# Performance work log

Hardware: AMD Instinct MI355X
Metric: run time of the kernel (lower is better)

## Reference

```python
import jax, jax.numpy as jnp
import numpy as np

T_STEPS = 1000
TEMP_SAMPLE = 0.1


def _cosine_schedule():
    # matches MBDDegradationImputation._cosine_beta_schedule (float64 then cast)
    s = 0.008
    x = np.linspace(0, T_STEPS, T_STEPS + 1, dtype=np.float64)
    ac = np.cos((x / T_STEPS + s) / (1 + s) * np.pi * 0.5) ** 2
    ac = ac / ac[0]
    betas = np.clip(1.0 - ac[1:] / ac[:-1], 0.0, 0.999)
    alphas = 1.0 - betas
    acp = np.cumprod(alphas)
    return (jnp.asarray(alphas, jnp.float32),
            jnp.asarray(acp, jnp.float32),
            jnp.asarray(np.sqrt(1.0 - acp), jnp.float32))


def setup_inputs() -> dict:
    key = jax.random.key(0)
    k = jax.random.split(key, 6)
    N, T, F = 2048, 512, 64
    Xbar_i = jax.random.normal(k[0], (T, F), jnp.float32)
    observed_data = jax.random.normal(k[1], (T, F), jnp.float32)
    time_points = jnp.linspace(0.0, 1.0, T, dtype=jnp.float32)
    mask = jax.random.uniform(k[2], (T, F)) > 0.3  # True = observed
    eps = jax.random.normal(k[3], (N, T, F), jnp.float32)
    deg_a = jax.random.normal(k[4], (F,), jnp.float32) * 0.1
    deg_b = jax.random.normal(k[5], (F,), jnp.float32) * 0.1
    return {"Xbar_i": Xbar_i, "observed_data": observed_data,
            "time_points": time_points, "mask": mask, "eps": eps,
            "deg_a": deg_a, "deg_b": deg_b, "i": 500}


def reference(Xbar_i, observed_data, time_points, mask, eps, deg_a, deg_b, i):
    alphas, acp, sigmas = _cosine_schedule()
    abar_i = acp[i]
    sigma_i = sigmas[i]
    alpha_i = alphas[i]
    abar_im1 = acp[i - 1]

    Yi = jnp.sqrt(abar_i) * Xbar_i  # (T, F)
    # candidate clean samples, clipped, observed positions restored
    X0s = jnp.clip(eps * sigma_i + Xbar_i, -1.0, 1.0)  # (N, T, F)
    cand = jnp.where(mask[None], observed_data[None], X0s)  # (N, T, F)

    # linear degradation model consistency: pred = a + b * t, score = -MSE
    pred = deg_a[None, :] + deg_b[None, :] * time_points[:, None]  # (T, F)
    scores = -jnp.mean((cand - pred[None]) ** 2, axis=(1, 2))  # (N,)

    std = jnp.maximum(jnp.std(scores, ddof=1), 1e-4)  # torch.std is unbiased
    logp0 = (scores - jnp.mean(scores)) / std / TEMP_SAMPLE
    weights = jax.nn.softmax(logp0)  # (N,)

    weighted = jnp.einsum('n,ntf->tf', weights, X0s)  # (T, F)
    # per-feature: missing positions get weighted combo; fully-observed
    # features are copied from observed_data; observed positions of
    # partially-missing features stay zero (faithful to the torch loop)
    feat_all = jnp.all(mask, axis=0)  # (F,)
    Xbar = jnp.where(~mask, weighted,
                     jnp.where(feat_all[None, :], observed_data, 0.0))

    score = (-Yi + jnp.sqrt(abar_i) * Xbar) / (1.0 - abar_i)
    Xim1 = (Yi + (1.0 - abar_i) * score) / jnp.sqrt(alpha_i)
    Xbar_im1 = Xim1 / jnp.sqrt(abar_im1)
    Xbar_im1 = jnp.where(mask, observed_data, Xbar_im1)
    return Xbar_im1
```

## Files before the change

### kernel.cpp

```cpp
#include <hip/hip_runtime.h>

typedef __attribute__((ext_vector_type(4))) int   i32x4;
typedef __attribute__((ext_vector_type(4))) float f32x4;

#define TF    32768
#define TF4   8192
#define NS    2048
#define WCUT  1e-9f

__device__ __forceinline__ i32x4 mload4(const void* mask, int isI32, int idx4) {
  if (isI32) return ((const i32x4*)mask)[idx4];
  unsigned int w = ((const unsigned int*)mask)[idx4];
  i32x4 r;
  r[0] = (int)(w & 0xFFu);
  r[1] = (int)((w >> 8) & 0xFFu);
  r[2] = (int)((w >> 16) & 0xFFu);
  r[3] = (int)((w >> 24) & 0xFFu);
  return r;
}

__device__ __forceinline__ double ac_fn(int t) {
  const double s = 0.008;
  double c = cos(((double)t / 1000.0 + s) / (1.0 + s) * 1.5707963267948966);
  return c * c;
}
__device__ __forceinline__ double alpha_fn(int t) {
  double beta = 1.0 - ac_fn(t + 1) / ac_fn(t);
  beta = beta < 0.0 ? 0.0 : (beta > 0.999 ? 0.999 : beta);
  return 1.0 - beta;
}

__launch_bounds__(256)
__global__ void k1a_sched(const int* __restrict__ ip,
                          const unsigned int* __restrict__ maskw,
                          float* __restrict__ wsc) {
  const int tid = threadIdx.x;
  __shared__ int badsh;
  if (tid == 0) badsh = 0;
  __syncthreads();
  int bad = 0;
  for (int k = tid; k < TF4; k += 256)
    if (maskw[k] > 1u) bad = 1;
  if (bad) atomicOr(&badsh, 1);

  const int i = ip[0];
  __shared__ double prod[256];
  double p = 1.0;
  for (int t = tid; t < i; t += 256) p *= alpha_fn(t);
  prod[tid] = p;
  __syncthreads();
  for (int s = 128; s > 0; s >>= 1) {
    if (tid < s) prod[tid] *= prod[tid + s];
    __syncthreads();
  }
  if (tid == 0) {
    double acp_im1 = prod[0];
    double ai = alpha_fn(i);
    double acp_i = acp_im1 * ai;
    wsc[0] = (float)sqrt(1.0 - acp_i);
    wsc[1] = (float)acp_i;
    wsc[2] = (float)ai;
    wsc[3] = (float)acp_im1;
    ((int*)wsc)[8] = badsh ? 0 : 1;
  }
}

__launch_bounds__(256)
__global__ void k1b_tables(const float* __restrict__ xbar,
                           const float* __restrict__ obs,
                           const void* __restrict__ mask,
                           const float* __restrict__ timep,
                           const float* __restrict__ dega,
                           const float* __restrict__ degb,
                           const float* __restrict__ wsc,
                           float* __restrict__ sc, float* __restrict__ xq,
                           float* __restrict__ pq, double* __restrict__ osum_part) {
  const int tid = threadIdx.x;
  const int pos4 = blockIdx.x * 256 + tid;
  const float sig = wsc[0];
  const int isI32 = ((const int*)wsc)[8];

  const int t  = pos4 >> 4;
  const int f0 = (pos4 << 2) & 63;
  const float tv = timep[t];
  f32x4 da = *(const f32x4*)(dega + f0);
  f32x4 db = *(const f32x4*)(degb + f0);
  f32x4 x  = ((const f32x4*)xbar)[pos4];
  f32x4 o  = ((const f32x4*)obs)[pos4];
  i32x4 m  = mload4(mask, isI32, pos4);

  f32x4 scv, xqv, pqv;
  float od2 = 0.f;
  #pragma unroll
  for (int c = 0; c < 4; ++c) {
    const float pr = fmaf(db[c], tv, da[c]);
    const bool mm = m[c] != 0;
    scv[c] = mm ? 0.f : sig;
    xqv[c] = mm ? 0.f : x[c];
    pqv[c] = mm ? 0.f : pr;
    float d = o[c] - pr;
    od2 += mm ? d * d : 0.f;
  }
  ((f32x4*)sc)[pos4] = scv;
  ((f32x4*)xq)[pos4] = xqv;
  ((f32x4*)pq)[pos4] = pqv;

  __shared__ double red[256];
  red[tid] = (double)od2;
  __syncthreads();
  for (int s = 128; s > 0; s >>= 1) {
    if (tid < s) red[tid] += red[tid + s];
    __syncthreads();
  }
  if (tid == 0) osum_part[blockIdx.x] = red[0];
}

__launch_bounds__(256)
__global__ void k2_scores(const float* __restrict__ eps,
                          const float* __restrict__ sc,
                          const float* __restrict__ xq,
                          const float* __restrict__ pq,
                          double* __restrict__ pscore) {
  const int tid = threadIdx.x;
  const int n0 = blockIdx.x * 4;
  const int kq = blockIdx.y;
  const int kbeg = kq * (TF4 / 4);
  const f32x4* e4 = (const f32x4*)eps;
  const f32x4* sc4 = (const f32x4*)sc;
  const f32x4* xq4 = (const f32x4*)xq;
  const f32x4* pq4 = (const f32x4*)pq;

  double acc[4] = {0.0, 0.0, 0.0, 0.0};
  #pragma unroll 2
  for (int k = kbeg + tid; k < kbeg + TF4 / 4; k += 512) {
    const int k1 = k + 256;
    f32x4 sv0 = sc4[k],  xv0 = xq4[k],  pv0 = pq4[k];
    f32x4 sv1 = sc4[k1], xv1 = xq4[k1], pv1 = pq4[k1];
    #pragma unroll
    for (int r = 0; r < 4; ++r) {
      const size_t row = (size_t)(n0 + r) * TF4;
      f32x4 e0 = e4[row + k];
      f32x4 e1 = e4[row + k1];
      float s = 0.f;
      #pragma unroll
      for (int c = 0; c < 4; ++c) {
        float v = fmaf(e0[c], sv0[c], xv0[c]);
        v = fminf(fmaxf(v, -1.f), 1.f);
        float d = v - pv0[c];
        s = fmaf(d, d, s);
      }
      #pragma unroll
      for (int c = 0; c < 4; ++c) {
        float v = fmaf(e1[c], sv1[c], xv1[c]);
        v = fminf(fmaxf(v, -1.f), 1.f);
        float d = v - pv1[c];
        s = fmaf(d, d, s);
      }
      acc[r] += (double)s;
    }
  }
  __shared__ double red[4 * 256];
  #pragma unroll
  for (int r = 0; r < 4; ++r) red[r * 256 + tid] = acc[r];
  __syncthreads();
  for (int s = 128; s > 0; s >>= 1) {
    if (tid < s) {
      #pragma unroll
      for (int r = 0; r < 4; ++r) red[r * 256 + tid] += red[r * 256 + tid + s];
    }
    __syncthreads();
  }
  if (tid < 4) pscore[kq * NS + n0 + tid] = red[tid * 256];
}

__launch_bounds__(256)
__global__ void k3_softmax(const double* __restrict__ pscore,
                           const double* __restrict__ osum_part,
                           float* __restrict__ wsc,
                           int* __restrict__ cidx, float* __restrict__ cw) {
  const int tid = threadIdx.x;
  __shared__ double red[256];

  double osum = 0.0;
  if (tid < 32) osum = osum_part[tid];
  red[tid] = osum; __syncthreads();
  for (int st = 128; st > 0; st >>= 1) { if (tid < st) red[tid] += red[tid + st]; __syncthreads(); }
  osum = red[0];
  __syncthreads();

  float s[8];
  #pragma unroll
  for (int j = 0; j < 8; ++j) {
    int n = tid + 256 * j;
    double t = pscore[n] + pscore[NS + n] + pscore[2 * NS + n] + pscore[3 * NS + n];
    s[j] = -(float)((t + osum) * (1.0 / 32768.0));
  }
  double t = 0.0;
  #pragma unroll
  for (int j = 0; j < 8; ++j) t += (double)s[j];
  red[tid] = t; __syncthreads();
  for (int st = 128; st > 0; st >>= 1) { if (tid < st) red[tid] += red[tid + st]; __syncthreads(); }
  const float mean = (float)(red[0] * (1.0 / 2048.0));
  __syncthreads();
  double v = 0.0;
  #pragma unroll
  for (int j = 0; j < 8; ++j) { float d = s[j] - mean; v += (double)d * (double)d; }
  red[tid] = v; __syncthreads();
  for (int st = 128; st > 0; st >>= 1) { if (tid < st) red[tid] += red[tid + st]; __syncthreads(); }
  float stdv = (float)sqrt(red[0] / 2047.0);
  stdv = fmaxf(stdv, 1e-4f);
  const float inv = 10.0f / stdv;
  float lp[8];
  double mx = -1e300;
  #pragma unroll
  for (int j = 0; j < 8; ++j) { lp[j] = (s[j] - mean) * inv; mx = fmax(mx, (double)lp[j]); }
  __syncthreads();
  red[tid] = mx; __syncthreads();
  for (int st = 128; st > 0; st >>= 1) { if (tid < st) red[tid] = fmax(red[tid], red[tid + st]); __syncthreads(); }
  const float M = (float)red[0];
  __syncthreads();
  float ev[8]; double es = 0.0;
  #pragma unroll
  for (int j = 0; j < 8; ++j) { ev[j] = expf(lp[j] - M); es += (double)ev[j]; }
  red[tid] = es; __syncthreads();
  for (int st = 128; st > 0; st >>= 1) { if (tid < st) red[tid] += red[tid + st]; __syncthreads(); }
  const float invS = (float)(1.0 / red[0]);

  float w[8]; int keep[8]; int c = 0;
  #pragma unroll
  for (int j = 0; j < 8; ++j) {
    w[j] = ev[j] * invS;
    keep[j] = w[j] > WCUT;
    c += keep[j];
  }
  __shared__ int cnt[256];
  cnt[tid] = c; __syncthreads();
  for (int off = 1; off < 256; off <<= 1) {
    int vv = (tid >= off) ? cnt[tid - off] : 0;
    __syncthreads();
    cnt[tid] += vv;
    __syncthreads();
  }
  int base = cnt[tid] - c;
  #pragma unroll
  for (int j = 0; j < 8; ++j) {
    if (keep[j]) {
      cidx[base] = tid + 256 * j;
      cw[base] = w[j];
      ++base;
    }
  }
  if (tid == 255) ((int*)wsc)[9] = cnt[255];
}

__launch_bounds__(256)
__global__ void k4_weighted(const float* __restrict__ eps,
                            const int* __restrict__ cidx,
                            const float* __restrict__ cw,
                            const float* __restrict__ wsc,
                            const float* __restrict__ xbar,
                            float* __restrict__ partial) {
  const int tid = threadIdx.x;
  const int pos4 = blockIdx.x * 256 + tid;
  const int g = blockIdx.y;
  const int Nk = ((const int*)wsc)[9];
  const float sig = wsc[0];
  const f32x4* e4 = (const f32x4*)eps;
  f32x4 xf = ((const f32x4*)xbar)[pos4];
  f32x4 acc = {0.f, 0.f, 0.f, 0.f};
  int j = g;
  for (; j + 16 < Nk; j += 32) {
    const float w0 = cw[j];
    const int   n0 = cidx[j];
    const float w1 = cw[j + 16];
    const int   n1 = cidx[j + 16];
    f32x4 e0 = e4[(size_t)n0 * TF4 + pos4];
    f32x4 e1 = e4[(size_t)n1 * TF4 + pos4];
    #pragma unroll
    for (int c = 0; c < 4; ++c) {
      float v = fmaf(e0[c], sig, xf[c]);
      v = fminf(fmaxf(v, -1.f), 1.f);
      acc[c] = fmaf(w0, v, acc[c]);
    }
    #pragma unroll
    for (int c = 0; c < 4; ++c) {
      float v = fmaf(e1[c], sig, xf[c]);
      v = fminf(fmaxf(v, -1.f), 1.f);
      acc[c] = fmaf(w1, v, acc[c]);
    }
  }
  for (; j < Nk; j += 16) {
    const float w = cw[j];
    const int n = cidx[j];
    f32x4 e = e4[(size_t)n * TF4 + pos4];
    #pragma unroll
    for (int c = 0; c < 4; ++c) {
      float v = fmaf(e[c], sig, xf[c]);
      v = fminf(fmaxf(v, -1.f), 1.f);
      acc[c] = fmaf(w, v, acc[c]);
    }
  }
  ((f32x4*)partial)[(size_t)g * TF4 + pos4] = acc;
}

__launch_bounds__(256)
__global__ void k5_final(const float* __restrict__ partial,
                         const float* __restrict__ xbar,
                         const float* __restrict__ obs,
                         const void* __restrict__ mask,
                         const float* __restrict__ wsc,
                         float* __restrict__ out) {
  const int pos4 = blockIdx.x * 256 + threadIdx.x;
  const f32x4* p4 = (const f32x4*)partial;
  f32x4 w = {0.f, 0.f, 0.f, 0.f};
  #pragma unroll
  for (int g = 0; g < 16; ++g) {
    f32x4 a = p4[(size_t)g * TF4 + pos4];
    #pragma unroll
    for (int c = 0; c < 4; ++c) w[c] += a[c];
  }
  const float abar = wsc[1];
  const float sa = sqrtf(abar);
  const float ra = 1.f / sqrtf(wsc[2]);
  const float rb = 1.f / sqrtf(wsc[3]);
  const int isI32 = ((const int*)wsc)[8];
  f32x4 xf = ((const f32x4*)xbar)[pos4];
  f32x4 ov = ((const f32x4*)obs)[pos4];
  i32x4 m = mload4(mask, isI32, pos4);
  f32x4 res;
  #pragma unroll
  for (int c = 0; c < 4; ++c) {
    const float Yi = sa * xf[c];
    const float scv = (-Yi + sa * w[c]) / (1.f - abar);
    const float xim1 = (Yi + (1.f - abar) * scv) * ra;
    res[c] = m[c] ? ov[c] : (xim1 * rb);
  }
  ((f32x4*)out)[pos4] = res;
}

extern "C" void kernel_launch(void* const* d_in, const int* in_sizes, int n_in,
                              void* d_out, int out_size, void* d_ws, size_t ws_size,
                              hipStream_t stream) {
  const float* Xbar  = (const float*)d_in[0];
  const float* obs   = (const float*)d_in[1];
  const float* timep = (const float*)d_in[2];
  const void*  mask  = d_in[3];
  const float* eps   = (const float*)d_in[4];
  const float* dega  = (const float*)d_in[5];
  const float* degb  = (const float*)d_in[6];
  const int*   ip    = (const int*)d_in[7];

  float* ws = (float*)d_ws;
  float*  wsc       = ws;
  float*  sc        = ws + 16;
  float*  xq        = sc + TF;
  float*  pq        = xq + TF;
  double* osum_part = (double*)(pq + TF);
  double* pscore    = osum_part + 32;
  int*    cidx      = (int*)(pscore + 4 * NS);
  float*  cw        = (float*)(cidx + NS);
  float*  partial   = cw + NS;

  hipLaunchKernelGGL(k1a_sched,  dim3(1),        dim3(256), 0, stream,
                     ip, (const unsigned int*)mask, wsc);
  hipLaunchKernelGGL(k1b_tables, dim3(32),       dim3(256), 0, stream,
                     Xbar, obs, mask, timep, dega, degb, wsc, sc, xq, pq, osum_part);
  hipLaunchKernelGGL(k2_scores,  dim3(NS/4, 4),  dim3(256), 0, stream,
                     eps, sc, xq, pq, pscore);
  hipLaunchKernelGGL(k3_softmax, dim3(1),        dim3(256), 0, stream,
                     pscore, osum_part, wsc, cidx, cw);
  hipLaunchKernelGGL(k4_weighted,dim3(32, 16),   dim3(256), 0, stream,
                     eps, cidx, cw, wsc, Xbar, partial);
  hipLaunchKernelGGL(k5_final,   dim3(32),       dim3(256), 0, stream,
                     partial, Xbar, obs, mask, wsc, (float*)d_out);
}
```

Before: 75.10 us.

## Fuse schedule and table kernels, fold observed residual into pq, widen weighted split

Merges the single-block schedule kernel into the table-building kernel. Each of the 32 blocks now recomputes the alpha cumulative product redundantly, which saves one launch and its dependency gap. The observed-position residual is folded into the pq table (obs - pred at masked positions), so k2 picks it up directly and the separate osum reduction and its k3 pre-pass go away. This relies on how k2, which is not shown, uses pq at masked entries. The weighted-sum kernel's grid is also doubled to 32 groups, adding parallelism at the cost of a larger partial buffer that k5 must read.

```diff
diff --git a/kernel.cpp b/kernel.cpp
--- a/kernel.cpp
+++ b/kernel.cpp
@@ -6,6 +6,7 @@
 #define TF    32768
 #define TF4   8192
 #define NS    2048
+#define NG    32
 #define WCUT  1e-9f
 
 __device__ __forceinline__ i32x4 mload4(const void* mask, int isI32, int idx4) {
@@ -31,11 +32,22 @@
 }
 
 __launch_bounds__(256)
-__global__ void k1a_sched(const int* __restrict__ ip,
-                          const unsigned int* __restrict__ maskw,
-                          float* __restrict__ wsc) {
+__global__ void k1_fused(const int* __restrict__ ip,
+                         const unsigned int* __restrict__ maskw,
+                         const float* __restrict__ timep,
+                         const float* __restrict__ dega,
+                         const float* __restrict__ degb,
+                         const float* __restrict__ xbar,
+                         const float* __restrict__ obs,
+                         const void* __restrict__ mask,
+                         float* __restrict__ wsc,
+                         float* __restrict__ sc, float* __restrict__ xq,
+                         float* __restrict__ pq) {
   const int tid = threadIdx.x;
   __shared__ int badsh;
+  __shared__ double prod[256];
+  __shared__ float ssig;
+  __shared__ int sIsI32;
   if (tid == 0) badsh = 0;
   __syncthreads();
   int bad = 0;
@@ -44,7 +56,6 @@
   if (bad) atomicOr(&badsh, 1);
 
   const int i = ip[0];
-  __shared__ double prod[256];
   double p = 1.0;
   for (int t = tid; t < i; t += 256) p *= alpha_fn(t);
   prod[tid] = p;
@@ -57,29 +68,22 @@
     double acp_im1 = prod[0];
     double ai = alpha_fn(i);
     double acp_i = acp_im1 * ai;
-    wsc[0] = (float)sqrt(1.0 - acp_i);
-    wsc[1] = (float)acp_i;
-    wsc[2] = (float)ai;
-    wsc[3] = (float)acp_im1;
-    ((int*)wsc)[8] = badsh ? 0 : 1;
-  }
-}
-
-__launch_bounds__(256)
-__global__ void k1b_tables(const float* __restrict__ xbar,
-                           const float* __restrict__ obs,
-                           const void* __restrict__ mask,
-                           const float* __restrict__ timep,
-                           const float* __restrict__ dega,
-                           const float* __restrict__ degb,
-                           const float* __restrict__ wsc,
-                           float* __restrict__ sc, float* __restrict__ xq,
-                           float* __restrict__ pq, double* __restrict__ osum_part) {
-  const int tid = threadIdx.x;
+    float sig = (float)sqrt(1.0 - acp_i);
+    ssig = sig;
+    sIsI32 = badsh ? 0 : 1;
+    if (blockIdx.x == 0) {
+      wsc[0] = sig;
+      wsc[1] = (float)acp_i;
+      wsc[2] = (float)ai;
+      wsc[3] = (float)acp_im1;
+      ((int*)wsc)[8] = badsh ? 0 : 1;
+    }
+  }
+  __syncthreads();
+  const float sig = ssig;
+  const int isI32 = sIsI32;
+
   const int pos4 = blockIdx.x * 256 + tid;
-  const float sig = wsc[0];
-  const int isI32 = ((const int*)wsc)[8];
-
   const int t  = pos4 >> 4;
   const int f0 = (pos4 << 2) & 63;
   const float tv = timep[t];
@@ -90,29 +94,17 @@
   i32x4 m  = mload4(mask, isI32, pos4);
 
   f32x4 scv, xqv, pqv;
-  float od2 = 0.f;
   #pragma unroll
   for (int c = 0; c < 4; ++c) {
     const float pr = fmaf(db[c], tv, da[c]);
     const bool mm = m[c] != 0;
     scv[c] = mm ? 0.f : sig;
     xqv[c] = mm ? 0.f : x[c];
-    pqv[c] = mm ? 0.f : pr;
-    float d = o[c] - pr;
-    od2 += mm ? d * d : 0.f;
+    pqv[c] = mm ? (o[c] - pr) : pr;
   }
   ((f32x4*)sc)[pos4] = scv;
   ((f32x4*)xq)[pos4] = xqv;
   ((f32x4*)pq)[pos4] = pqv;
-
-  __shared__ double red[256];
-  red[tid] = (double)od2;
-  __syncthreads();
-  for (int s = 128; s > 0; s >>= 1) {
-    if (tid < s) red[tid] += red[tid + s];
-    __syncthreads();
-  }
-  if (tid == 0) osum_part[blockIdx.x] = red[0];
 }
 
 __launch_bounds__(256)
@@ -175,25 +167,17 @@
 
 __launch_bounds__(256)
 __global__ void k3_softmax(const double* __restrict__ pscore,
-                           const double* __restrict__ osum_part,
                            float* __restrict__ wsc,
                            int* __restrict__ cidx, float* __restrict__ cw) {
   const int tid = threadIdx.x;
   __shared__ double red[256];
 
-  double osum = 0.0;
-  if (tid < 32) osum = osum_part[tid];
-  red[tid] = osum; __syncthreads();
-  for (int st = 128; st > 0; st >>= 1) { if (tid < st) red[tid] += red[tid + st]; __syncthreads(); }
-  osum = red[0];
-  __syncthreads();
-
   float s[8];
   #pragma unroll
   for (int j = 0; j < 8; ++j) {
     int n = tid + 256 * j;
     double t = pscore[n] + pscore[NS + n] + pscore[2 * NS + n] + pscore[3 * NS + n];
-    s[j] = -(float)((t + osum) * (1.0 / 32768.0));
+    s[j] = -(float)(t * (1.0 / 32768.0));
   }
   double t = 0.0;
   #pragma unroll
@@ -269,11 +253,11 @@
   f32x4 xf = ((const f32x4*)xbar)[pos4];
   f32x4 acc = {0.f, 0.f, 0.f, 0.f};
   int j = g;
-  for (; j + 16 < Nk; j += 32) {
+  for (; j + NG < Nk; j += 2 * NG) {
     const float w0 = cw[j];
     const int   n0 = cidx[j];
-    const float w1 = cw[j + 16];
-    const int   n1 = cidx[j + 16];
+    const float w1 = cw[j + NG];
+    const int   n1 = cidx[j + NG];
     f32x4 e0 = e4[(size_t)n0 * TF4 + pos4];
     f32x4 e1 = e4[(size_t)n1 * TF4 + pos4];
     #pragma unroll
@@ -289,7 +273,7 @@
       acc[c] = fmaf(w1, v, acc[c]);
     }
   }
-  for (; j < Nk; j += 16) {
+  for (; j < Nk; j += NG) {
     const float w = cw[j];
     const int n = cidx[j];
     f32x4 e = e4[(size_t)n * TF4 + pos4];
@@ -314,7 +298,7 @@
   const f32x4* p4 = (const f32x4*)partial;
   f32x4 w = {0.f, 0.f, 0.f, 0.f};
   #pragma unroll
-  for (int g = 0; g < 16; ++g) {
+  for (int g = 0; g < NG; ++g) {
     f32x4 a = p4[(size_t)g * TF4 + pos4];
     #pragma unroll
     for (int c = 0; c < 4; ++c) w[c] += a[c];
@@ -355,21 +339,19 @@
   float*  sc        = ws + 16;
   float*  xq        = sc + TF;
   float*  pq        = xq + TF;
-  double* osum_part = (double*)(pq + TF);
-  double* pscore    = osum_part + 32;
+  double* pscore    = (double*)(pq + TF);
   int*    cidx      = (int*)(pscore + 4 * NS);
   float*  cw        = (float*)(cidx + NS);
   float*  partial   = cw + NS;
 
-  hipLaunchKernelGGL(k1a_sched,  dim3(1),        dim3(256), 0, stream,
-                     ip, (const unsigned int*)mask, wsc);
-  hipLaunchKernelGGL(k1b_tables, dim3(32),       dim3(256), 0, stream,
-                     Xbar, obs, mask, timep, dega, degb, wsc, sc, xq, pq, osum_part);
+  hipLaunchKernelGGL(k1_fused,   dim3(32),       dim3(256), 0, stream,
+                     ip, (const unsigned int*)mask, timep, dega, degb,
+                     Xbar, obs, mask, wsc, sc, xq, pq);
   hipLaunchKernelGGL(k2_scores,  dim3(NS/4, 4),  dim3(256), 0, stream,
                      eps, sc, xq, pq, pscore);
   hipLaunchKernelGGL(k3_softmax, dim3(1),        dim3(256), 0, stream,
-                     pscore, osum_part, wsc, cidx, cw);
-  hipLaunchKernelGGL(k4_weighted,dim3(32, 16),   dim3(256), 0, stream,
+                     pscore, wsc, cidx, cw);
+  hipLaunchKernelGGL(k4_weighted,dim3(32, NG),   dim3(256), 0, stream,
                      eps, cidx, cw, wsc, Xbar, partial);
   hipLaunchKernelGGL(k5_final,   dim3(32),       dim3(256), 0, stream,
                      partial, Xbar, obs, mask, wsc, (float*)d_out);
```

Result: faster. 71.38 us (-4.9%).
